# Performance work log

Hardware: AMD Instinct MI355X
Metric: run time of the kernel (lower is better)

Reference implementation:

```python
import jax, jax.numpy as jnp
import numpy as np

# cls_loss defaults from DetectionLoss.cls_loss
ALPHA = 0.75
GAMMA = 2.0
NUM_NEG = 10000   # negatives randomly subsampled per sample
NUM_HARD = 100    # hard negatives kept when there are no positives
RATIO = 100       # neg:pos hard-mining ratio

B = 8
N = 64 * 128 * 128  # anchor points for crop_size=[64,128,128]


def setup_inputs() -> dict:
    key = jax.random.key(0)
    k1, k2, k3, k4 = jax.random.split(key, 4)
    # logits, biased negative so sigmoid ~ small background prob
    pred = jax.random.normal(k1, (B, N, 1), jnp.float32) * 2.0 - 4.0
    # sparse binary targets: ~50 positive voxels per sample
    target = (jax.random.uniform(k2, (B, N, 1)) < 5e-5).astype(jnp.float32)
    # ignore mask: 0 = use, -1 = ignore (as written by target_proprocess)
    mask_ignore = -(jax.random.uniform(k3, (B, N, 1)) < 1e-3).astype(jnp.float32)
    # deterministic replacement for random.sample over negative indices:
    # per-sample random permutation prefix (without replacement)
    perm = jax.vmap(lambda k: jax.random.permutation(k, N)[:NUM_NEG])(
        jax.random.split(k4, B))
    return {"pred": pred, "target": target, "mask_ignore": mask_ignore,
            "neg_idx": perm.astype(jnp.int32)}


def _per_sample_loss(pred_b, target_b, mask_b, idx):
    # pred_b/target_b/mask_b: (N,1); idx: (NUM_NEG,)
    pred_b = pred_b[:, 0]
    target_b = target_b[:, 0]
    mask_b = mask_b[:, 0]
    # focal weight uses detached probabilities (pred_b.detach() in torch)
    prob = jnp.clip(jax.nn.sigmoid(jax.lax.stop_gradient(pred_b)), 1e-4, 1.0 - 1e-4)
    pos = target_b == 1.0
    alpha_f = jnp.where(pos, ALPHA, 1.0 - ALPHA)
    focal_w = alpha_f * jnp.where(pos, 1.0 - prob, prob) ** GAMMA
    # numerically stable BCE-with-logits, reduction='none'
    bce = jnp.maximum(pred_b, 0.0) - pred_b * target_b + jnp.log1p(jnp.exp(-jnp.abs(pred_b)))
    loss = jnp.where(mask_b == 0.0, focal_w * bce, 0.0)
    # false-negative boost (only positives can match, so safe unconditionally)
    loss = jnp.where(pos & (prob < 0.8), 4.0 * loss, loss)

    num_pos = jnp.sum(pos)
    pos_sum = jnp.sum(jnp.where(pos, loss, 0.0))

    # gather the NUM_NEG randomly subsampled candidates; mask out any index
    # that accidentally hits a positive with sentinel -1 (losses are >= 0)
    neg_vals = jnp.where(pos[idx], -1.0, loss[idx])          # (NUM_NEG,)
    sorted_desc = jnp.sort(neg_vals)[::-1]                    # descending
    # k = min(ratio*num_pos, NUM_NEG) if positives exist else NUM_HARD
    k = jnp.where(num_pos > 0, jnp.minimum(RATIO * num_pos, NUM_NEG), NUM_HARD)
    keep = (jnp.arange(NUM_NEG) < k) & (sorted_desc >= 0.0)
    neg_sum = jnp.sum(jnp.where(keep, sorted_desc, 0.0))

    return (pos_sum + neg_sum) / jnp.maximum(num_pos.astype(jnp.float32), 1.0)


def reference(pred, target, mask_ignore, neg_idx):
    losses = jax.vmap(_per_sample_loss)(pred, target, mask_ignore, neg_idx)
    return jnp.mean(losses)
```

## Files before the change

kernel.cpp:

```cpp
#include <hip/hip_runtime.h>
#include <math.h>

namespace {

constexpr float kAlpha   = 0.75f;
constexpr int   kNumNeg  = 10000;
constexpr int   kNumHard = 100;
constexpr int   kRatio   = 100;
constexpr int   kB       = 8;
constexpr int   kN       = 64 * 128 * 128;
constexpr int   kBlocksPerB = 128;
constexpr int   kPosBlocks  = kB * kBlocksPerB;
constexpr int   kGatherBlocks = (kB * kNumNeg + 255) / 256;
constexpr int   kTpb1    = 256;
constexpr int   kTpbSel  = 1024;
constexpr int   kWavesSel = kTpbSel / 64;
constexpr int   kVPerThread = (kNumNeg + kTpbSel - 1) / kTpbSel;
constexpr unsigned kSentinel = 0xFFFFFFFFu;

__device__ __forceinline__ float loss_at(float pred, float target, float mask) {
    float prob = 1.0f / (1.0f + expf(-pred));
    prob = fminf(fmaxf(prob, 1.0e-4f), 1.0f - 1.0e-4f);
    bool pos = (target == 1.0f);
    float alpha_f = pos ? kAlpha : (1.0f - kAlpha);
    float pt = pos ? (1.0f - prob) : prob;
    float focal_w = alpha_f * pt * pt;
    float bce = fmaxf(pred, 0.0f) - pred * target + log1pf(expf(-fabsf(pred)));
    float loss = (mask == 0.0f) ? focal_w * bce : 0.0f;
    if (pos && prob < 0.8f) loss *= 4.0f;
    return loss;
}

__global__ void __launch_bounds__(kTpb1) stage1_kernel(
        const float* __restrict__ pred, const float* __restrict__ target,
        const float* __restrict__ mask, const int* __restrict__ neg_idx,
        float* __restrict__ partials, unsigned* __restrict__ gvals,
        unsigned* __restrict__ counter) {
    const int blk = blockIdx.x;
    if (blk == 0 && threadIdx.x == 0) *counter = 0u;

    if (blk < kPosBlocks) {
        const int b = blk >> 7;
        const int slice = blk & 127;
        const size_t base = (size_t)b * kN;
        const float4* t4 = (const float4*)(target + base);
        const int nvec = kN / 4;

        float cnt = 0.0f, psum = 0.0f;
        for (int i = slice * kTpb1 + threadIdx.x; i < nvec; i += kTpb1 * kBlocksPerB) {
            float4 tv = t4[i];
            float tvv[4] = {tv.x, tv.y, tv.z, tv.w};
            #pragma unroll
            for (int c = 0; c < 4; ++c) {
                if (tvv[c] == 1.0f) {
                    int gi = i * 4 + c;
                    cnt += 1.0f;
                    psum += loss_at(pred[base + gi], 1.0f, mask[base + gi]);
                }
            }
        }
        #pragma unroll
        for (int off = 32; off > 0; off >>= 1) {
            cnt  += __shfl_down(cnt, off);
            psum += __shfl_down(psum, off);
        }
        __shared__ float sc[kTpb1 / 64], sp[kTpb1 / 64];
        const int wave = threadIdx.x / 64, lane = threadIdx.x % 64;
        if (lane == 0) { sc[wave] = cnt; sp[wave] = psum; }
        __syncthreads();
        if (threadIdx.x == 0) {
            float c = 0.0f, p = 0.0f;
            for (int w = 0; w < kTpb1 / 64; ++w) { c += sc[w]; p += sp[w]; }
            float* slot = partials + ((size_t)b * kBlocksPerB + slice) * 2;
            slot[0] = c; slot[1] = p;
        }
    } else {
        const int t = (blk - kPosBlocks) * kTpb1 + threadIdx.x;
        if (t < kB * kNumNeg) {
            const int b = t / kNumNeg;
            const int j = t - b * kNumNeg;
            const size_t base = (size_t)b * kN;
            const int gi = neg_idx[(size_t)b * kNumNeg + j];
            const float tg = target[base + gi];
            unsigned outv;
            if (tg == 1.0f) {
                outv = kSentinel;
            } else {
                float v = loss_at(pred[base + gi], tg, mask[base + gi]);
                outv = __float_as_uint(v);
            }
            gvals[(size_t)b * kNumNeg + j] = outv;
        }
    }
}

__global__ void __launch_bounds__(kTpbSel) select_kernel(
        const unsigned* __restrict__ gvals, const float* __restrict__ partials,
        float* __restrict__ batch_loss, unsigned* __restrict__ counter,
        float* __restrict__ out) {
    __shared__ unsigned whist[kWavesSel][256];
    __shared__ unsigned hist_total[256];
    __shared__ unsigned sfx[256];
    __shared__ float r0[kWavesSel], r1[kWavesSel], r2[kWavesSel], r3[kWavesSel];
    __shared__ float red[kWavesSel];
    __shared__ float sh_np, sh_ps;
    __shared__ unsigned sh_krem, sh_prefix;
    __shared__ int sh_done;

    const int b = blockIdx.x;
    const int tid = threadIdx.x;
    const int wave = tid >> 6, lane = tid & 63;

    for (int i = tid; i < kWavesSel * 256; i += kTpbSel)
        ((unsigned*)whist)[i] = 0u;
    __syncthreads();

    unsigned vreg[kVPerThread];
    float mcnt = 0.0f, msum = 0.0f;
    #pragma unroll
    for (int it = 0; it < kVPerThread; ++it) {
        const int j = tid + it * kTpbSel;
        unsigned v = kSentinel;
        if (j < kNumNeg) v = gvals[(size_t)b * kNumNeg + j];
        vreg[it] = v;
        if (v != kSentinel) {
            mcnt += 1.0f;
            msum += __uint_as_float(v);
            atomicAdd(&whist[wave][v >> 24], 1u);
        }
    }
    float c = 0.0f, p = 0.0f;
    if (tid < kBlocksPerB) {
        const float* slot = partials + ((size_t)b * kBlocksPerB + tid) * 2;
        c = slot[0]; p = slot[1];
    }
    #pragma unroll
    for (int off = 32; off > 0; off >>= 1) {
        mcnt += __shfl_down(mcnt, off);
        msum += __shfl_down(msum, off);
        c    += __shfl_down(c, off);
        p    += __shfl_down(p, off);
    }
    if (lane == 0) { r0[wave] = mcnt; r1[wave] = msum; r2[wave] = c; r3[wave] = p; }
    __syncthreads();
    float my_loss = 0.0f;
    if (tid == 0) {
        float a0 = 0, a1 = 0, a2 = 0, a3 = 0;
        for (int w = 0; w < kWavesSel; ++w) { a0 += r0[w]; a1 += r1[w]; a2 += r2[w]; a3 += r3[w]; }
        sh_np = a2; sh_ps = a3;
        const int num_pos = (int)a2;
        const int m = (int)a0;
        const int k = (num_pos > 0) ? min(kRatio * num_pos, kNumNeg) : kNumHard;
        if (k >= m) {
            my_loss = (a3 + a1) / fmaxf(a2, 1.0f);
            sh_done = 1;
        } else {
            sh_done = 0;
            sh_krem = (unsigned)k;
            sh_prefix = 0u;
        }
    }
    __syncthreads();

    if (!sh_done) {
        #pragma unroll
        for (int pass = 0; pass < 4; ++pass) {
            const int shift = 24 - 8 * pass;
            if (pass > 0) {
                for (int i = tid; i < kWavesSel * 256; i += kTpbSel)
                    ((unsigned*)whist)[i] = 0u;
                __syncthreads();
                const unsigned pmask = 0xFFFFFFFFu << (shift + 8);
                const unsigned pval = sh_prefix;
                #pragma unroll
                for (int it = 0; it < kVPerThread; ++it) {
                    unsigned v = vreg[it];
                    if (v != kSentinel && (v & pmask) == pval)
                        atomicAdd(&whist[wave][(v >> shift) & 255u], 1u);
                }
            }
            __syncthreads();
            if (tid < 256) {
                unsigned h = 0;
                #pragma unroll
                for (int w = 0; w < kWavesSel; ++w) h += whist[w][tid];
                hist_total[tid] = h;
            }
            __syncthreads();
            if (wave == 0) {
                unsigned v0 = hist_total[255 - (4 * lane + 0)];
                unsigned v1 = hist_total[255 - (4 * lane + 1)];
                unsigned v2 = hist_total[255 - (4 * lane + 2)];
                unsigned v3 = hist_total[255 - (4 * lane + 3)];
                unsigned p0 = v0, p1 = p0 + v1, p2 = p1 + v2, p3 = p2 + v3;
                unsigned acc = p3;
                #pragma unroll
                for (int off = 1; off < 64; off <<= 1) {
                    unsigned y = __shfl_up(acc, off);
                    if (lane >= off) acc += y;
                }
                unsigned excl = acc - p3;
                sfx[255 - (4 * lane + 0)] = excl + p0;
                sfx[255 - (4 * lane + 1)] = excl + p1;
                sfx[255 - (4 * lane + 2)] = excl + p2;
                sfx[255 - (4 * lane + 3)] = excl + p3;
            }
            __syncthreads();
            const unsigned krem = sh_krem;
            __syncthreads();
            if (tid < 256) {
                unsigned si = sfx[tid];
                bool sel = (si >= krem) && (tid == 255 || sfx[tid + 1] < krem);
                if (sel) {
                    sh_krem = krem - (si - hist_total[tid]);
                    sh_prefix |= (unsigned)tid << shift;
                }
            }
            __syncthreads();
        }

        const unsigned tbits = sh_prefix;
        float gsum = 0.0f;
        #pragma unroll
        for (int it = 0; it < kVPerThread; ++it) {
            unsigned v = vreg[it];
            if (v != kSentinel && v > tbits) gsum += __uint_as_float(v);
        }
        #pragma unroll
        for (int off = 32; off > 0; off >>= 1) gsum += __shfl_down(gsum, off);
        if (lane == 0) red[wave] = gsum;
        __syncthreads();
        if (tid == 0) {
            float sum_gt = 0.0f;
            for (int w = 0; w < kWavesSel; ++w) sum_gt += red[w];
            const float tval = __uint_as_float(sh_prefix);
            const float neg_sum = sum_gt + (float)sh_krem * tval;
            my_loss = (sh_ps + neg_sum) / fmaxf(sh_np, 1.0f);
        }
    }

    if (tid == 0) {
        __hip_atomic_store(&batch_loss[b], my_loss, __ATOMIC_RELEASE,
                           __HIP_MEMORY_SCOPE_AGENT);
        unsigned old = __hip_atomic_fetch_add(counter, 1u, __ATOMIC_ACQ_REL,
                                              __HIP_MEMORY_SCOPE_AGENT);
        if (old == (unsigned)(kB - 1)) {
            float s = 0.0f;
            for (int i = 0; i < kB; ++i)
                s += __hip_atomic_load(&batch_loss[i], __ATOMIC_ACQUIRE,
                                       __HIP_MEMORY_SCOPE_AGENT);
            out[0] = s / (float)kB;
        }
    }
}

}

extern "C" void kernel_launch(void* const* d_in, const int* in_sizes, int n_in,
                              void* d_out, int out_size, void* d_ws, size_t ws_size,
                              hipStream_t stream) {
    const float* pred   = (const float*)d_in[0];
    const float* target = (const float*)d_in[1];
    const float* mask   = (const float*)d_in[2];
    const int*   negidx = (const int*)d_in[3];
    float* ws = (float*)d_ws;
    float*    partials   = ws;
    float*    batch_loss = ws + 2048;
    unsigned* counter    = (unsigned*)(ws + 2056);
    unsigned* gvals      = (unsigned*)(ws + 2064);
    float* out = (float*)d_out;

    stage1_kernel<<<dim3(kPosBlocks + kGatherBlocks), dim3(kTpb1), 0, stream>>>(
        pred, target, mask, negidx, partials, gvals, counter);
    select_kernel<<<dim3(kB), dim3(kTpbSel), 0, stream>>>(
        gvals, partials, batch_loss, counter, out);
}
```

Before: 30.28 us.

## Fuse stage1 and select kernels into one launch with flag-based inter-block sync

Merges the positive-scan/gather kernel and the per-sample radix-select kernel into a single launch. Select blocks spin on magic-value flags in workspace until the gather and positive-partial blocks have published their results, and block 0 waits on per-sample loss flags to write the final mean. Block counts and sizes also change to 1024-thread blocks with fewer slices. This removes a kernel launch boundary at the cost of an extra memset and a reliance on all blocks being co-resident to avoid deadlock.

```diff
diff --git a/kernel.cpp b/kernel.cpp
--- a/kernel.cpp
+++ b/kernel.cpp
@@ -9,14 +9,22 @@
 constexpr int   kRatio   = 100;
 constexpr int   kB       = 8;
 constexpr int   kN       = 64 * 128 * 128;
-constexpr int   kBlocksPerB = 128;
-constexpr int   kPosBlocks  = kB * kBlocksPerB;
-constexpr int   kGatherBlocks = (kB * kNumNeg + 255) / 256;
-constexpr int   kTpb1    = 256;
-constexpr int   kTpbSel  = 1024;
-constexpr int   kWavesSel = kTpbSel / 64;
-constexpr int   kVPerThread = (kNumNeg + kTpbSel - 1) / kTpbSel;
+constexpr int   kSlices  = 24;
+constexpr int   kPosBlocks    = kB * kSlices;
+constexpr int   kGatherBlocks = 56;
+constexpr int   kGrid    = kPosBlocks + kGatherBlocks + kB;
+constexpr int   kTpb     = 1024;
+constexpr int   kWaves   = kTpb / 64;
+constexpr int   kVPer    = (kNumNeg + kTpb - 1) / kTpb;
 constexpr unsigned kSentinel = 0xFFFFFFFFu;
+constexpr unsigned kMagic    = 0x13579BDFu;
+
+constexpr int oPartials    = 0;
+constexpr int oBatchLoss   = 512;
+constexpr int oPosFlags    = 1024;
+constexpr int oGatherFlags = 1280;
+constexpr int oLossFlags   = 1408;
+constexpr int oGvals       = 1536;
 
 __device__ __forceinline__ float loss_at(float pred, float target, float mask) {
     float prob = 1.0f / (1.0f + expf(-pred));
@@ -31,23 +39,31 @@
     return loss;
 }
 
-__global__ void __launch_bounds__(kTpb1) stage1_kernel(
+__device__ __forceinline__ unsigned flag_load(const unsigned* p) {
+    return __hip_atomic_load(p, __ATOMIC_ACQUIRE, __HIP_MEMORY_SCOPE_AGENT);
+}
+__device__ __forceinline__ void flag_store(unsigned* p, unsigned v) {
+    __hip_atomic_store(p, v, __ATOMIC_RELEASE, __HIP_MEMORY_SCOPE_AGENT);
+}
+
+__global__ void __launch_bounds__(kTpb, 4) fused_kernel(
         const float* __restrict__ pred, const float* __restrict__ target,
         const float* __restrict__ mask, const int* __restrict__ neg_idx,
-        float* __restrict__ partials, unsigned* __restrict__ gvals,
-        unsigned* __restrict__ counter) {
+        unsigned* __restrict__ ws, float* __restrict__ out) {
     const int blk = blockIdx.x;
-    if (blk == 0 && threadIdx.x == 0) *counter = 0u;
+    const int tid = threadIdx.x;
+    const int wave = tid >> 6, lane = tid & 63;
+    float* wsf = (float*)ws;
 
     if (blk < kPosBlocks) {
-        const int b = blk >> 7;
-        const int slice = blk & 127;
+        const int b = blk & 7;
+        const int slice = blk >> 3;
         const size_t base = (size_t)b * kN;
         const float4* t4 = (const float4*)(target + base);
         const int nvec = kN / 4;
 
         float cnt = 0.0f, psum = 0.0f;
-        for (int i = slice * kTpb1 + threadIdx.x; i < nvec; i += kTpb1 * kBlocksPerB) {
+        for (int i = slice * kTpb + tid; i < nvec; i += kSlices * kTpb) {
             float4 tv = t4[i];
             float tvv[4] = {tv.x, tv.y, tv.z, tv.w};
             #pragma unroll
@@ -64,23 +80,24 @@
             cnt  += __shfl_down(cnt, off);
             psum += __shfl_down(psum, off);
         }
-        __shared__ float sc[kTpb1 / 64], sp[kTpb1 / 64];
-        const int wave = threadIdx.x / 64, lane = threadIdx.x % 64;
+        __shared__ float sc[kWaves], sp[kWaves];
         if (lane == 0) { sc[wave] = cnt; sp[wave] = psum; }
         __syncthreads();
-        if (threadIdx.x == 0) {
+        if (tid == 0) {
             float c = 0.0f, p = 0.0f;
-            for (int w = 0; w < kTpb1 / 64; ++w) { c += sc[w]; p += sp[w]; }
-            float* slot = partials + ((size_t)b * kBlocksPerB + slice) * 2;
-            slot[0] = c; slot[1] = p;
-        }
-    } else {
-        const int t = (blk - kPosBlocks) * kTpb1 + threadIdx.x;
-        if (t < kB * kNumNeg) {
-            const int b = t / kNumNeg;
-            const int j = t - b * kNumNeg;
-            const size_t base = (size_t)b * kN;
-            const int gi = neg_idx[(size_t)b * kNumNeg + j];
+            for (int w = 0; w < kWaves; ++w) { c += sc[w]; p += sp[w]; }
+            wsf[oPartials + 2 * blk]     = c;
+            wsf[oPartials + 2 * blk + 1] = p;
+            __threadfence();
+            flag_store(&ws[oPosFlags + blk], kMagic);
+        }
+    } else if (blk < kPosBlocks + kGatherBlocks) {
+        const int g = blk - kPosBlocks;
+        for (int t = g * kTpb + tid; t < kB * kNumNeg; t += kGatherBlocks * kTpb) {
+            const int b2 = t / kNumNeg;
+            const int j  = t - b2 * kNumNeg;
+            const size_t base = (size_t)b2 * kN;
+            const int gi = neg_idx[(size_t)b2 * kNumNeg + j];
             const float tg = target[base + gi];
             unsigned outv;
             if (tg == 1.0f) {
@@ -89,167 +106,177 @@
                 float v = loss_at(pred[base + gi], tg, mask[base + gi]);
                 outv = __float_as_uint(v);
             }
-            gvals[(size_t)b * kNumNeg + j] = outv;
-        }
-    }
-}
-
-__global__ void __launch_bounds__(kTpbSel) select_kernel(
-        const unsigned* __restrict__ gvals, const float* __restrict__ partials,
-        float* __restrict__ batch_loss, unsigned* __restrict__ counter,
-        float* __restrict__ out) {
-    __shared__ unsigned whist[kWavesSel][256];
-    __shared__ unsigned hist_total[256];
-    __shared__ unsigned sfx[256];
-    __shared__ float r0[kWavesSel], r1[kWavesSel], r2[kWavesSel], r3[kWavesSel];
-    __shared__ float red[kWavesSel];
-    __shared__ float sh_np, sh_ps;
-    __shared__ unsigned sh_krem, sh_prefix;
-    __shared__ int sh_done;
-
-    const int b = blockIdx.x;
-    const int tid = threadIdx.x;
-    const int wave = tid >> 6, lane = tid & 63;
-
-    for (int i = tid; i < kWavesSel * 256; i += kTpbSel)
-        ((unsigned*)whist)[i] = 0u;
-    __syncthreads();
-
-    unsigned vreg[kVPerThread];
-    float mcnt = 0.0f, msum = 0.0f;
-    #pragma unroll
-    for (int it = 0; it < kVPerThread; ++it) {
-        const int j = tid + it * kTpbSel;
-        unsigned v = kSentinel;
-        if (j < kNumNeg) v = gvals[(size_t)b * kNumNeg + j];
-        vreg[it] = v;
-        if (v != kSentinel) {
-            mcnt += 1.0f;
-            msum += __uint_as_float(v);
-            atomicAdd(&whist[wave][v >> 24], 1u);
-        }
-    }
-    float c = 0.0f, p = 0.0f;
-    if (tid < kBlocksPerB) {
-        const float* slot = partials + ((size_t)b * kBlocksPerB + tid) * 2;
-        c = slot[0]; p = slot[1];
-    }
-    #pragma unroll
-    for (int off = 32; off > 0; off >>= 1) {
-        mcnt += __shfl_down(mcnt, off);
-        msum += __shfl_down(msum, off);
-        c    += __shfl_down(c, off);
-        p    += __shfl_down(p, off);
-    }
-    if (lane == 0) { r0[wave] = mcnt; r1[wave] = msum; r2[wave] = c; r3[wave] = p; }
-    __syncthreads();
-    float my_loss = 0.0f;
-    if (tid == 0) {
-        float a0 = 0, a1 = 0, a2 = 0, a3 = 0;
-        for (int w = 0; w < kWavesSel; ++w) { a0 += r0[w]; a1 += r1[w]; a2 += r2[w]; a3 += r3[w]; }
-        sh_np = a2; sh_ps = a3;
-        const int num_pos = (int)a2;
-        const int m = (int)a0;
-        const int k = (num_pos > 0) ? min(kRatio * num_pos, kNumNeg) : kNumHard;
-        if (k >= m) {
-            my_loss = (a3 + a1) / fmaxf(a2, 1.0f);
-            sh_done = 1;
-        } else {
-            sh_done = 0;
-            sh_krem = (unsigned)k;
-            sh_prefix = 0u;
-        }
-    }
-    __syncthreads();
-
-    if (!sh_done) {
-        #pragma unroll
-        for (int pass = 0; pass < 4; ++pass) {
-            const int shift = 24 - 8 * pass;
-            if (pass > 0) {
-                for (int i = tid; i < kWavesSel * 256; i += kTpbSel)
-                    ((unsigned*)whist)[i] = 0u;
-                __syncthreads();
-                const unsigned pmask = 0xFFFFFFFFu << (shift + 8);
-                const unsigned pval = sh_prefix;
-                #pragma unroll
-                for (int it = 0; it < kVPerThread; ++it) {
-                    unsigned v = vreg[it];
-                    if (v != kSentinel && (v & pmask) == pval)
-                        atomicAdd(&whist[wave][(v >> shift) & 255u], 1u);
-                }
-            }
+            ws[oGvals + t] = outv;
+        }
+        __syncthreads();
+        if (tid == 0) {
+            __threadfence();
+            flag_store(&ws[oGatherFlags + g], kMagic);
+        }
+    } else {
+        const int b = blk - (kPosBlocks + kGatherBlocks);
+        __shared__ unsigned whist[kWaves][256];
+        __shared__ unsigned hist_total[256], sfx[256];
+        __shared__ float r0[kWaves], r1[kWaves], red[kWaves];
+        __shared__ float sh_np, sh_ps;
+        __shared__ unsigned sh_krem, sh_prefix;
+        __shared__ int sh_done;
+
+        for (int i = tid; i < kWaves * 256; i += kTpb)
+            ((unsigned*)whist)[i] = 0u;
+        __syncthreads();
+
+        if (tid < kGatherBlocks) {
+            while (flag_load(&ws[oGatherFlags + tid]) != kMagic)
+                __builtin_amdgcn_s_sleep(8);
+        }
+        __syncthreads();
+
+        unsigned vreg[kVPer];
+        float mcnt = 0.0f, msum = 0.0f;
+        #pragma unroll
+        for (int it = 0; it < kVPer; ++it) {
+            const int j = tid + it * kTpb;
+            unsigned v = kSentinel;
+            if (j < kNumNeg) v = ws[oGvals + b * kNumNeg + j];
+            vreg[it] = v;
+            if (v != kSentinel) {
+                mcnt += 1.0f;
+                msum += __uint_as_float(v);
+                atomicAdd(&whist[wave][v >> 24], 1u);
+            }
+        }
+        #pragma unroll
+        for (int off = 32; off > 0; off >>= 1) {
+            mcnt += __shfl_down(mcnt, off);
+            msum += __shfl_down(msum, off);
+        }
+        if (lane == 0) { r0[wave] = mcnt; r1[wave] = msum; }
+
+        float c = 0.0f, p = 0.0f;
+        if (tid < kSlices) {
+            const int pb = tid * 8 + b;
+            while (flag_load(&ws[oPosFlags + pb]) != kMagic)
+                __builtin_amdgcn_s_sleep(8);
+            c = wsf[oPartials + 2 * pb];
+            p = wsf[oPartials + 2 * pb + 1];
+        }
+        #pragma unroll
+        for (int off = 32; off > 0; off >>= 1) {
+            c += __shfl_down(c, off);
+            p += __shfl_down(p, off);
+        }
+        __syncthreads();
+
+        float my_loss = 0.0f;
+        if (tid == 0) {
+            float a0 = 0.0f, a1 = 0.0f;
+            for (int w = 0; w < kWaves; ++w) { a0 += r0[w]; a1 += r1[w]; }
+            sh_np = c; sh_ps = p;
+            const int num_pos = (int)c;
+            const int m = (int)a0;
+            const int k = (num_pos > 0) ? min(kRatio * num_pos, kNumNeg) : kNumHard;
+            if (k >= m) {
+                my_loss = (p + a1) / fmaxf(c, 1.0f);
+                sh_done = 1;
+            } else {
+                sh_done = 0;
+                sh_krem = (unsigned)k;
+                sh_prefix = 0u;
+            }
+        }
+        __syncthreads();
+
+        if (!sh_done) {
+            #pragma unroll
+            for (int pass = 0; pass < 4; ++pass) {
+                const int shift = 24 - 8 * pass;
+                if (pass > 0) {
+                    for (int i = tid; i < kWaves * 256; i += kTpb)
+                        ((unsigned*)whist)[i] = 0u;
+                    __syncthreads();
+                    const unsigned pmask = 0xFFFFFFFFu << (shift + 8);
+                    const unsigned pval = sh_prefix;
+                    #pragma unroll
+                    for (int it = 0; it < kVPer; ++it) {
+                        unsigned v = vreg[it];
+                        if (v != kSentinel && (v & pmask) == pval)
+                            atomicAdd(&whist[wave][(v >> shift) & 255u], 1u);
+                    }
+                }
+                __syncthreads();
+                if (tid < 256) {
+                    unsigned h = 0;
+                    #pragma unroll
+                    for (int w = 0; w < kWaves; ++w) h += whist[w][tid];
+                    hist_total[tid] = h;
+                }
+                __syncthreads();
+                if (wave == 0) {
+                    unsigned v0 = hist_total[255 - (4 * lane + 0)];
+                    unsigned v1 = hist_total[255 - (4 * lane + 1)];
+                    unsigned v2 = hist_total[255 - (4 * lane + 2)];
+                    unsigned v3 = hist_total[255 - (4 * lane + 3)];
+                    unsigned p0 = v0, p1 = p0 + v1, p2 = p1 + v2, p3 = p2 + v3;
+                    unsigned acc = p3;
+                    #pragma unroll
+                    for (int off = 1; off < 64; off <<= 1) {
+                        unsigned y = __shfl_up(acc, off);
+                        if (lane >= off) acc += y;
+                    }
+                    unsigned excl = acc - p3;
+                    sfx[255 - (4 * lane + 0)] = excl + p0;
+                    sfx[255 - (4 * lane + 1)] = excl + p1;
+                    sfx[255 - (4 * lane + 2)] = excl + p2;
+                    sfx[255 - (4 * lane + 3)] = excl + p3;
+                }
+                __syncthreads();
+                const unsigned krem = sh_krem;
+                __syncthreads();
+                if (tid < 256) {
+                    unsigned si = sfx[tid];
+                    bool sel = (si >= krem) && (tid == 255 || sfx[tid + 1] < krem);
+                    if (sel) {
+                        sh_krem = krem - (si - hist_total[tid]);
+                        sh_prefix |= (unsigned)tid << shift;
+                    }
+                }
+                __syncthreads();
+            }
+
+            const unsigned tbits = sh_prefix;
+            float gsum = 0.0f;
+            #pragma unroll
+            for (int it = 0; it < kVPer; ++it) {
+                unsigned v = vreg[it];
+                if (v != kSentinel && v > tbits) gsum += __uint_as_float(v);
+            }
+            #pragma unroll
+            for (int off = 32; off > 0; off >>= 1) gsum += __shfl_down(gsum, off);
+            if (lane == 0) red[wave] = gsum;
             __syncthreads();
-            if (tid < 256) {
-                unsigned h = 0;
-                #pragma unroll
-                for (int w = 0; w < kWavesSel; ++w) h += whist[w][tid];
-                hist_total[tid] = h;
-            }
-            __syncthreads();
-            if (wave == 0) {
-                unsigned v0 = hist_total[255 - (4 * lane + 0)];
-                unsigned v1 = hist_total[255 - (4 * lane + 1)];
-                unsigned v2 = hist_total[255 - (4 * lane + 2)];
-                unsigned v3 = hist_total[255 - (4 * lane + 3)];
-                unsigned p0 = v0, p1 = p0 + v1, p2 = p1 + v2, p3 = p2 + v3;
-                unsigned acc = p3;
-                #pragma unroll
-                for (int off = 1; off < 64; off <<= 1) {
-                    unsigned y = __shfl_up(acc, off);
-                    if (lane >= off) acc += y;
-                }
-                unsigned excl = acc - p3;
-                sfx[255 - (4 * lane + 0)] = excl + p0;
-                sfx[255 - (4 * lane + 1)] = excl + p1;
-                sfx[255 - (4 * lane + 2)] = excl + p2;
-                sfx[255 - (4 * lane + 3)] = excl + p3;
-            }
-            __syncthreads();
-            const unsigned krem = sh_krem;
-            __syncthreads();
-            if (tid < 256) {
-                unsigned si = sfx[tid];
-                bool sel = (si >= krem) && (tid == 255 || sfx[tid + 1] < krem);
-                if (sel) {
-                    sh_krem = krem - (si - hist_total[tid]);
-                    sh_prefix |= (unsigned)tid << shift;
-                }
-            }
-            __syncthreads();
-        }
-
-        const unsigned tbits = sh_prefix;
-        float gsum = 0.0f;
-        #pragma unroll
-        for (int it = 0; it < kVPerThread; ++it) {
-            unsigned v = vreg[it];
-            if (v != kSentinel && v > tbits) gsum += __uint_as_float(v);
-        }
-        #pragma unroll
-        for (int off = 32; off > 0; off >>= 1) gsum += __shfl_down(gsum, off);
-        if (lane == 0) red[wave] = gsum;
-        __syncthreads();
-        if (tid == 0) {
-            float sum_gt = 0.0f;
-            for (int w = 0; w < kWavesSel; ++w) sum_gt += red[w];
-            const float tval = __uint_as_float(sh_prefix);
-            const float neg_sum = sum_gt + (float)sh_krem * tval;
-            my_loss = (sh_ps + neg_sum) / fmaxf(sh_np, 1.0f);
-        }
-    }
-
-    if (tid == 0) {
-        __hip_atomic_store(&batch_loss[b], my_loss, __ATOMIC_RELEASE,
-                           __HIP_MEMORY_SCOPE_AGENT);
-        unsigned old = __hip_atomic_fetch_add(counter, 1u, __ATOMIC_ACQ_REL,
-                                              __HIP_MEMORY_SCOPE_AGENT);
-        if (old == (unsigned)(kB - 1)) {
-            float s = 0.0f;
-            for (int i = 0; i < kB; ++i)
-                s += __hip_atomic_load(&batch_loss[i], __ATOMIC_ACQUIRE,
-                                       __HIP_MEMORY_SCOPE_AGENT);
-            out[0] = s / (float)kB;
+            if (tid == 0) {
+                float sum_gt = 0.0f;
+                for (int w = 0; w < kWaves; ++w) sum_gt += red[w];
+                const float tval = __uint_as_float(sh_prefix);
+                const float neg_sum = sum_gt + (float)sh_krem * tval;
+                my_loss = (sh_ps + neg_sum) / fmaxf(sh_np, 1.0f);
+            }
+        }
+
+        if (tid == 0) {
+            wsf[oBatchLoss + b] = my_loss;
+            __threadfence();
+            flag_store(&ws[oLossFlags + b], kMagic);
+            if (b == 0) {
+                float s = 0.0f;
+                for (int i = 0; i < kB; ++i) {
+                    while (flag_load(&ws[oLossFlags + i]) != kMagic)
+                        __builtin_amdgcn_s_sleep(8);
+                    s += wsf[oBatchLoss + i];
+                }
+                out[0] = s / (float)kB;
+            }
         }
     }
 }
@@ -263,15 +290,10 @@
     const float* target = (const float*)d_in[1];
     const float* mask   = (const float*)d_in[2];
     const int*   negidx = (const int*)d_in[3];
-    float* ws = (float*)d_ws;
-    float*    partials   = ws;
-    float*    batch_loss = ws + 2048;
-    unsigned* counter    = (unsigned*)(ws + 2056);
-    unsigned* gvals      = (unsigned*)(ws + 2064);
+    unsigned* ws = (unsigned*)d_ws;
     float* out = (float*)d_out;
 
-    stage1_kernel<<<dim3(kPosBlocks + kGatherBlocks), dim3(kTpb1), 0, stream>>>(
-        pred, target, mask, negidx, partials, gvals, counter);
-    select_kernel<<<dim3(kB), dim3(kTpbSel), 0, stream>>>(
-        gvals, partials, batch_loss, counter, out);
-}
+    hipMemsetAsync((char*)d_ws + oPosFlags * 4, 0, (oGvals - oPosFlags) * 4, stream);
+    fused_kernel<<<dim3(kGrid), dim3(kTpb), 0, stream>>>(pred, target, mask,
+                                                         negidx, ws, out);
+}
```

New measurement: 47.99 us. 1.58x slower.
